# Kernel tuning notes

Hardware: AMD Instinct MI355X
Metric: run time of the kernel (lower is better)

The kernel has to match this reference:

```python
import jax, jax.numpy as jnp
import numpy as np

H = 64      # hidden width of each MLP
M_STEPS = 64   # SDE steps (m)
N_SIM = 2048   # Monte-Carlo paths (n)
D = 128        # number of options (data_size)


def _mlp4(x, W1, b1, W2, b2, W3, b3):
    # x: [n, d, 4]; weights stacked over the 4 networks on axis 0 (k)
    h = jax.nn.relu(jnp.einsum('ndf,kfh->kndh', x, W1) + b1[:, None, None, :])
    h = jax.nn.relu(jnp.einsum('kndh,khg->kndg', h, W2) + b2[:, None, None, :])
    o = jnp.einsum('kndg,kgo->kndo', h, W3) + b3[:, None, None, :]
    return jnp.tanh(o)  # [4, n, d, 1]


def setup_inputs() -> dict:
    key = jax.random.key(0)
    ks = jax.random.split(key, 12)
    S0 = jax.random.uniform(ks[0], (D,), jnp.float32, 50.0, 150.0)
    K = jax.random.uniform(ks[1], (D,), jnp.float32, 50.0, 150.0)
    T = jax.random.uniform(ks[2], (D,), jnp.float32, 0.25, 2.0)
    rf = jnp.array([0.03], jnp.float32)
    V0 = jnp.array([0.04], jnp.float32)
    rho = jnp.array([-0.5], jnp.float32)
    Z1 = jax.random.normal(ks[3], (M_STEPS, N_SIM, D), jnp.float32)
    Z2raw = jax.random.normal(ks[4], (M_STEPS, N_SIM, D), jnp.float32)
    # 4 MLPs, layers [4, H, H, 1]
    W1 = jax.random.normal(ks[5], (4, 4, H), jnp.float32) / jnp.sqrt(4.0)
    b1 = jnp.zeros((4, H), jnp.float32)
    W2 = jax.random.normal(ks[6], (4, H, H), jnp.float32) / jnp.sqrt(float(H))
    b2 = jnp.zeros((4, H), jnp.float32)
    W3 = jax.random.normal(ks[7], (4, H, 1), jnp.float32) / jnp.sqrt(float(H))
    b3 = jnp.zeros((4, 1), jnp.float32)
    return {"S0": S0, "K": K, "T": T, "rf": rf, "V0": V0, "rho": rho,
            "Z1": Z1, "Z2raw": Z2raw,
            "W1": W1, "b1": b1, "W2": W2, "b2": b2, "W3": W3, "b3": b3}


def reference(S0, K, T, rf, V0, rho, Z1, Z2raw, W1, b1, W2, b2, W3, b3):
    m, n, d = Z1.shape
    dt = (T / m)[None, :, None]          # [1, d, 1]
    sdt = jnp.sqrt(dt)
    rho_s = rho[0]
    rf_s = rf[0]
    S = jnp.broadcast_to(S0[None, :, None], (n, d, 1))
    V = jnp.broadcast_to(V0[0], (n, d, 1))

    def step(carry, xs):
        S, V = carry
        j, z1, z2r = xs                    # z1, z2r: [n, d]
        z2 = rho_s * z1 + jnp.sqrt(1.0 - rho_s ** 2) * z2r
        feat = jnp.concatenate([
            S, V,
            jnp.broadcast_to(rf_s, S.shape),
            jnp.broadcast_to(dt * j, S.shape),
        ], axis=2)                          # [n, d, 4]
        N1, N2, N3, N4 = _mlp4(feat, W1, b1, W2, b2, W3, b3)
        Vn = V * (1.0 + N3 * dt + N4 * sdt * z2[..., None])
        Sn = S * (1.0 + N1 * dt + N2 * sdt * z1[..., None])
        return (Sn, Vn), None

    js = jnp.arange(m, dtype=jnp.float32)
    (S, V), _ = jax.lax.scan(step, (S, V), (js, Z1, Z2raw))
    S = S[..., 0]                            # [n, d]
    payoff = jnp.maximum(S - K[None, :], 0.0)
    P_pred = jnp.sum(jnp.exp(-rf_s * T)[None, :] * payoff, axis=0) / n
    return P_pred
```

## Files before the change

kernel.cpp:

```cpp
#include <hip/hip_runtime.h>
#include <math.h>

#define D_OPT   128
#define N_SIM   2048
#define M_STEPS 64
#define HID     64


typedef _Float16 f16x8 __attribute__((ext_vector_type(8)));
typedef _Float16 f16x4 __attribute__((ext_vector_type(4)));
typedef _Float16 f16x2 __attribute__((ext_vector_type(2)));
typedef float    f32x4 __attribute__((ext_vector_type(4)));
typedef unsigned int u32;
typedef u32 u32x2 __attribute__((ext_vector_type(2)));
typedef u32 u32x4 __attribute__((ext_vector_type(4)));

__device__ __forceinline__ u32 pk2u(float a, float b) {
#if __has_builtin(__builtin_amdgcn_cvt_pkrtz)
    return __builtin_bit_cast(u32, __builtin_amdgcn_cvt_pkrtz(a, b));
#else
    f16x2 p; p[0] = (_Float16)a; p[1] = (_Float16)b;
    return __builtin_bit_cast(u32, p);
#endif
}

__device__ __forceinline__ u32 pk_relu_cvt(float a, float b) {
    f16x2 p = __builtin_bit_cast(f16x2, pk2u(a, b));
    const f16x2 z = { (_Float16)0.0f, (_Float16)0.0f };
#if __has_builtin(__builtin_elementwise_max)
    p = __builtin_elementwise_max(p, z);
#else
    p[0] = p[0] > z[0] ? p[0] : z[0];
    p[1] = p[1] > z[1] ? p[1] : z[1];
#endif
    return __builtin_bit_cast(u32, p);
}

__global__ __launch_bounds__(256, 4) void nsde_kernel(
    const float* __restrict__ S0p, const float* __restrict__ Kp,
    const float* __restrict__ Tp,  const float* __restrict__ rfp,
    const float* __restrict__ V0p, const float* __restrict__ rhop,
    const float* __restrict__ Z1,  const float* __restrict__ Z2r,
    const float* __restrict__ W1,  const float* __restrict__ B1,
    const float* __restrict__ W2,  const float* __restrict__ B2,
    const float* __restrict__ W3,  const float* __restrict__ B3,
    float* __restrict__ out)
{
    __shared__ float nvp[2][4][64];
    __shared__ u32x2 pkx[4][64];

    const int tid  = threadIdx.x;
    const int wave = tid >> 6;
    const int lane = tid & 63;
    const int q    = lane >> 4;
    const int mA   = lane & 15;
    const float rf = rfp[0];

    const float* w1g = W1 + wave * 256;
    const float* b1g = B1 + wave * 64;
    const float* w2g = W2 + wave * 4096;
    const float* b2g = B2 + wave * 64;
    const float* w3g = W3 + wave * 64;

    f16x4 A1[4];
    #pragma unroll
    for (int t = 0; t < 4; ++t) {
        f16x4 a = { (_Float16)0.0f, (_Float16)0.0f, (_Float16)0.0f, (_Float16)0.0f };
        if (q == 0) {
            const int h = t * 16 + mA;
            a[0] = (_Float16)w1g[0 * 64 + h];
            a[1] = (_Float16)w1g[1 * 64 + h];
            a[2] = (_Float16)w1g[3 * 64 + h];
            a[3] = (_Float16)fmaf(rf, w1g[2 * 64 + h], b1g[h]);
        }
        A1[t] = a;
    }

    f16x8 A2[4][2];
    #pragma unroll
    for (int gt = 0; gt < 4; ++gt)
        #pragma unroll
        for (int kt = 0; kt < 2; ++kt) {
            f16x8 a;
            #pragma unroll
            for (int j = 0; j < 8; ++j) {
                const int h1 = (2 * kt + (j >> 2)) * 16 + 4 * q + (j & 3);
                a[j] = (_Float16)w2g[h1 * 64 + gt * 16 + mA];
            }
            A2[gt][kt] = a;
        }

    f16x8 A3[2];
    #pragma unroll
    for (int kt = 0; kt < 2; ++kt) {
        f16x8 a;
        #pragma unroll
        for (int j = 0; j < 8; ++j) a[j] = (_Float16)0.0f;
        if (mA == 0) {
            #pragma unroll
            for (int j = 0; j < 8; ++j) {
                const int g = (2 * kt + (j >> 2)) * 16 + 4 * q + (j & 3);
                a[j] = (_Float16)w3g[g];
            }
        }
        A3[kt] = a;
    }

    f32x4 cinit2[4];
    #pragma unroll
    for (int t = 0; t < 4; ++t)
        #pragma unroll
        for (int r = 0; r < 4; ++r)
            cinit2[t][r] = b2g[t * 16 + 4 * q + r];
    const f32x4 zc = { 0.0f, 0.0f, 0.0f, 0.0f };

    const float b3n0 = B3[0], b3n1 = B3[1], b3n2 = B3[2], b3n3 = B3[3];

    const int ebase = blockIdx.x * 64;
    const int d_own = (ebase + lane) & (D_OPT - 1);
    const float dt_own  = Tp[d_own] * (1.0f / (float)M_STEPS);
    const float sdt_own = sqrtf(dt_own);

    float Sreg = S0p[d_own];
    float Vreg = V0p[0];
    {
        u32x2 pk0;
        pk0[0] = pk2u(Sreg, Vreg);
        pk0[1] = pk2u(0.0f, 1.0f);
        pkx[wave][lane] = pk0;
    }

    const float rho   = rhop[0];
    const float rho_c = sqrtf(1.0f - rho * rho);
    const size_t estep = (size_t)N_SIM * D_OPT;
    const float* z1p = Z1  + (size_t)ebase + (size_t)lane;
    const float* z2p = Z2r + (size_t)ebase + (size_t)lane;

    #pragma unroll 1
    for (int s = 0; s < M_STEPS; ++s) {
        const float z1  = *z1p;
        const float z2r = *z2p;
        z1p += estep; z2p += estep;

        #pragma unroll 2
        for (int mt = 0; mt < 4; ++mt) {
            const u32x2 pksv = pkx[wave][mt * 16 + mA];
            const f16x4 B1f = __builtin_bit_cast(f16x4, pksv);

            u32x4 b2u[2];
            #pragma unroll
            for (int t = 0; t < 4; ++t) {
                const f32x4 acc = __builtin_amdgcn_mfma_f32_16x16x16f16(
                                      A1[t], B1f, zc, 0, 0, 0);
                b2u[t >> 1][(t & 1) * 2 + 0] = pk_relu_cvt(acc[0], acc[1]);
                b2u[t >> 1][(t & 1) * 2 + 1] = pk_relu_cvt(acc[2], acc[3]);
            }
            const f16x8 B2f0 = __builtin_bit_cast(f16x8, b2u[0]);
            const f16x8 B2f1 = __builtin_bit_cast(f16x8, b2u[1]);

            u32x4 b3u[2];
            #pragma unroll
            for (int gt = 0; gt < 4; ++gt) {
                f32x4 acc = __builtin_amdgcn_mfma_f32_16x16x32_f16(
                                A2[gt][0], B2f0, cinit2[gt], 0, 0, 0);
                acc = __builtin_amdgcn_mfma_f32_16x16x32_f16(
                                A2[gt][1], B2f1, acc, 0, 0, 0);
                b3u[gt >> 1][(gt & 1) * 2 + 0] = pk_relu_cvt(acc[0], acc[1]);
                b3u[gt >> 1][(gt & 1) * 2 + 1] = pk_relu_cvt(acc[2], acc[3]);
            }

            f32x4 acc3 = __builtin_amdgcn_mfma_f32_16x16x32_f16(
                             A3[0], __builtin_bit_cast(f16x8, b3u[0]), zc, 0, 0, 0);
            acc3 = __builtin_amdgcn_mfma_f32_16x16x32_f16(
                             A3[1], __builtin_bit_cast(f16x8, b3u[1]), acc3, 0, 0, 0);

            if (q == 0)
                nvp[s & 1][wave][mt * 16 + mA] = acc3[0];
        }

        __syncthreads();

        {
            const float o0 = nvp[s & 1][0][lane] + b3n0;
            const float o1 = nvp[s & 1][1][lane] + b3n1;
            const float o2 = nvp[s & 1][2][lane] + b3n2;
            const float o3 = nvp[s & 1][3][lane] + b3n3;
            const float e0 = __expf(2.0f * o0);
            const float e1 = __expf(2.0f * o1);
            const float e2 = __expf(2.0f * o2);
            const float e3 = __expf(2.0f * o3);
            const float N0 = 1.0f - 2.0f / (e0 + 1.0f);
            const float N1 = 1.0f - 2.0f / (e1 + 1.0f);
            const float N2 = 1.0f - 2.0f / (e2 + 1.0f);
            const float N3 = 1.0f - 2.0f / (e3 + 1.0f);
            const float z2 = fmaf(rho, z1, rho_c * z2r);
            const float fS = fmaf(N1 * sdt_own, z1, N0 * dt_own);
            const float fV = fmaf(N3 * sdt_own, z2, N2 * dt_own);
            Sreg = fmaf(Sreg, fS, Sreg);
            Vreg = fmaf(Vreg, fV, Vreg);
            u32x2 pkn;
            pkn[0] = pk2u(Sreg, Vreg);
            pkn[1] = pk2u(dt_own * (float)(s + 1), 1.0f);
            pkx[wave][lane] = pkn;
        }
    }

    if (wave == 0) {
        const float Td  = dt_own * (float)M_STEPS;
        const float pay = fmaxf(Sreg - Kp[d_own], 0.0f);
        atomicAdd(&out[d_own], __expf(-rf * Td) * pay * (1.0f / (float)N_SIM));
    }
}

extern "C" void kernel_launch(void* const* d_in, const int* in_sizes, int n_in,
                              void* d_out, int out_size, void* d_ws, size_t ws_size,
                              hipStream_t stream)
{
    const float* S0  = (const float*)d_in[0];
    const float* K   = (const float*)d_in[1];
    const float* T   = (const float*)d_in[2];
    const float* rf  = (const float*)d_in[3];
    const float* V0  = (const float*)d_in[4];
    const float* rho = (const float*)d_in[5];
    const float* Z1  = (const float*)d_in[6];
    const float* Z2r = (const float*)d_in[7];
    const float* W1  = (const float*)d_in[8];
    const float* B1  = (const float*)d_in[9];
    const float* W2  = (const float*)d_in[10];
    const float* B2  = (const float*)d_in[11];
    const float* W3  = (const float*)d_in[12];
    const float* B3  = (const float*)d_in[13];
    float* out = (float*)d_out;

    hipMemsetAsync(out, 0, (size_t)out_size * sizeof(float), stream);

    const int total = N_SIM * D_OPT;
    const int grid  = total / 64;
    nsde_kernel<<<grid, 256, 0, stream>>>(S0, K, T, rf, V0, rho, Z1, Z2r,
                                          W1, B1, W2, B2, W3, B3, out);
}
```

Baseline: 817.8 us.

## Replace LDS state exchange with ds_bpermute and prefetch noise one step ahead

```diff
diff --git a/kernel.cpp b/kernel.cpp
--- a/kernel.cpp
+++ b/kernel.cpp
@@ -47,7 +47,6 @@
     float* __restrict__ out)
 {
     __shared__ float nvp[2][4][64];
-    __shared__ u32x2 pkx[4][64];
 
     const int tid  = threadIdx.x;
     const int wave = tid >> 6;
@@ -121,14 +120,16 @@
     const float dt_own  = Tp[d_own] * (1.0f / (float)M_STEPS);
     const float sdt_own = sqrtf(dt_own);
 
+    float dtf_[4], dts_[4];
+    #pragma unroll
+    for (int mt = 0; mt < 4; ++mt) {
+        dtf_[mt] = Tp[(ebase + mt * 16 + mA) & (D_OPT - 1)] * (1.0f / (float)M_STEPS);
+        dts_[mt] = 0.0f;
+    }
+
     float Sreg = S0p[d_own];
     float Vreg = V0p[0];
-    {
-        u32x2 pk0;
-        pk0[0] = pk2u(Sreg, Vreg);
-        pk0[1] = pk2u(0.0f, 1.0f);
-        pkx[wave][lane] = pk0;
-    }
+    u32 pkSV = pk2u(Sreg, Vreg);
 
     const float rho   = rhop[0];
     const float rho_c = sqrtf(1.0f - rho * rho);
@@ -136,22 +137,36 @@
     const float* z1p = Z1  + (size_t)ebase + (size_t)lane;
     const float* z2p = Z2r + (size_t)ebase + (size_t)lane;
 
+    float z1c = *z1p;
+    float z2c = *z2p;
+    z1p += estep; z2p += estep;
+
+    const int pbase = mA * 4;
+
     #pragma unroll 1
     for (int s = 0; s < M_STEPS; ++s) {
-        const float z1  = *z1p;
-        const float z2r = *z2p;
-        z1p += estep; z2p += estep;
+        const float z1n = *z1p;
+        const float z2n = *z2p;
+        const size_t adv = (s < M_STEPS - 2) ? estep : (size_t)0;
+        z1p += adv; z2p += adv;
+
+        f16x4 B1f_[4];
+        #pragma unroll
+        for (int mt = 0; mt < 4; ++mt) {
+            u32x2 b;
+            b[0] = (u32)__builtin_amdgcn_ds_bpermute(pbase + mt * 64, (int)pkSV);
+            b[1] = pk2u(dts_[mt], 1.0f);
+            B1f_[mt] = __builtin_bit_cast(f16x4, b);
+            dts_[mt] += dtf_[mt];
+        }
 
         #pragma unroll 2
         for (int mt = 0; mt < 4; ++mt) {
-            const u32x2 pksv = pkx[wave][mt * 16 + mA];
-            const f16x4 B1f = __builtin_bit_cast(f16x4, pksv);
-
             u32x4 b2u[2];
             #pragma unroll
             for (int t = 0; t < 4; ++t) {
                 const f32x4 acc = __builtin_amdgcn_mfma_f32_16x16x16f16(
-                                      A1[t], B1f, zc, 0, 0, 0);
+                                      A1[t], B1f_[mt], zc, 0, 0, 0);
                 b2u[t >> 1][(t & 1) * 2 + 0] = pk_relu_cvt(acc[0], acc[1]);
                 b2u[t >> 1][(t & 1) * 2 + 1] = pk_relu_cvt(acc[2], acc[3]);
             }
@@ -178,7 +193,7 @@
                 nvp[s & 1][wave][mt * 16 + mA] = acc3[0];
         }
 
-        __syncthreads();
+        asm volatile("s_waitcnt lgkmcnt(0)\n\ts_barrier" ::: "memory");
 
         {
             const float o0 = nvp[s & 1][0][lane] + b3n0;
@@ -193,15 +208,13 @@
             const float N1 = 1.0f - 2.0f / (e1 + 1.0f);
             const float N2 = 1.0f - 2.0f / (e2 + 1.0f);
             const float N3 = 1.0f - 2.0f / (e3 + 1.0f);
-            const float z2 = fmaf(rho, z1, rho_c * z2r);
-            const float fS = fmaf(N1 * sdt_own, z1, N0 * dt_own);
+            const float z2 = fmaf(rho, z1c, rho_c * z2c);
+            const float fS = fmaf(N1 * sdt_own, z1c, N0 * dt_own);
             const float fV = fmaf(N3 * sdt_own, z2, N2 * dt_own);
             Sreg = fmaf(Sreg, fS, Sreg);
             Vreg = fmaf(Vreg, fV, Vreg);
-            u32x2 pkn;
-            pkn[0] = pk2u(Sreg, Vreg);
-            pkn[1] = pk2u(dt_own * (float)(s + 1), 1.0f);
-            pkx[wave][lane] = pkn;
+            pkSV = pk2u(Sreg, Vreg);
+            z1c = z1n; z2c = z2n;
         }
     }
 
```

After: 1.449 ms. +77.2%, slower.
